# Optimization experiments

Measured on AMD Instinct MI355X. Metric: run time of the kernel, lower is better.

The kernel has to match this reference:

```python
import jax, jax.numpy as jnp
import numpy as np

B, N, H, HS, PH = 8, 384, 12, 768, 64
D = HS // H  # 64


def _ln(x, g, b, eps=1e-5):
    m = jnp.mean(x, axis=-1, keepdims=True)
    v = jnp.mean(jnp.square(x - m), axis=-1, keepdims=True)
    return (x - m) * jax.lax.rsqrt(v + eps) * g + b


def setup_inputs() -> dict:
    key = jax.random.key(0)
    ks = jax.random.split(key, 16)
    s = 0.02
    return {
        "nodes": jax.random.normal(ks[0], (B, N, HS), jnp.float32),
        "bias": jnp.zeros((B, 1, 1, N), jnp.float32),
        "paths": jax.random.normal(ks[1], (B, N, N, PH), jnp.float32),
        "Wq": jax.random.normal(ks[2], (HS, HS), jnp.float32) * s,
        "bq": jnp.zeros((HS,), jnp.float32),
        "Wk": jax.random.normal(ks[3], (HS, HS), jnp.float32) * s,
        "bk": jnp.zeros((HS,), jnp.float32),
        "Wv": jax.random.normal(ks[4], (HS, HS), jnp.float32) * s,
        "bv": jnp.zeros((HS,), jnp.float32),
        "Wsk": jax.random.normal(ks[5], (PH, D), jnp.float32) * s,
        "bsk": jnp.zeros((D,), jnp.float32),
        "Wsv": jax.random.normal(ks[6], (PH, D), jnp.float32) * s,
        "bsv": jnp.zeros((D,), jnp.float32),
        "Wo": jax.random.normal(ks[7], (HS, HS), jnp.float32) * s,
        "bo": jnp.zeros((HS,), jnp.float32),
        "ln_g": jnp.ones((HS,), jnp.float32),
        "ln_b": jnp.zeros((HS,), jnp.float32),
        "pln_g": jnp.ones((PH,), jnp.float32),
        "pln_b": jnp.zeros((PH,), jnp.float32),
    }


def reference(nodes, bias, paths, Wq, bq, Wk, bk, Wv, bv, Wsk, bsk, Wsv, bsv,
              Wo, bo, ln_g, ln_b, pln_g, pln_b):
    # q/k/v projections, split heads -> (B, H, N, D)
    def split(x):
        return x.reshape(B, N, H, D).transpose(0, 2, 1, 3)

    q = split(nodes @ Wq + bq)
    k = split(nodes @ Wk + bk)
    v = split(nodes @ Wv + bv)

    p = _ln(paths, pln_g, pln_b)            # (B, N, N, PH)
    struct_k = p @ Wsk + bsk                # (B, N, N, D)
    struct_v = p @ Wsv + bsv                # (B, N, N, D)

    q = q * (D ** -0.5)
    w = jnp.einsum('bhid,bhjd->bhij', q, k)           # content scores
    w = w + jnp.einsum('bhid,bijd->bhij', q, struct_k)  # structural scores
    w = jax.nn.softmax(w + bias, axis=-1)             # (B, H, N, N)

    out = jnp.einsum('bhij,bhjd->bhid', w, v) \
        + jnp.einsum('bhij,bijd->bhid', w, struct_v)  # (B, H, N, D)
    out = out.transpose(0, 2, 1, 3).reshape(B, N, HS)
    out = jax.nn.relu(out @ Wo + bo)
    # dropout p=0.0 -> identity
    return _ln(nodes + out, ln_g, ln_b), w
```

## Files before the change

### kernel.cpp

```cpp
#include <hip/hip_runtime.h>
#include <hip/hip_bf16.h>

typedef __hip_bfloat16 bf16;
typedef __attribute__((ext_vector_type(8))) short short8b;
typedef __attribute__((ext_vector_type(4))) float f32x4;

#define BB  8
#define NN  384
#define HH  12
#define HSZ 768
#define DD  64
#define PHH 64
#define PSTR 386
#define SWS  194

__device__ __forceinline__ float bflo(unsigned u){ union{unsigned q; float f;} c; c.q = u << 16;        return c.f; }
__device__ __forceinline__ float bfhi(unsigned u){ union{unsigned q; float f;} c; c.q = u & 0xffff0000u; return c.f; }

__device__ __forceinline__ unsigned pk2bf(float lo, float hi){
    union{float f; unsigned u;} a, b; a.f = lo; b.f = hi;
    unsigned ua = a.u + 0x7fffu + ((a.u >> 16) & 1u);
    unsigned ub = b.u + 0x7fffu + ((b.u >> 16) & 1u);
    return (ua >> 16) | (ub & 0xffff0000u);
}

union U8 { uint4 u; short8b v; };

__device__ __forceinline__ void pk32(const float4* p, uint4* o){
    #pragma unroll
    for (int e = 0; e < 4; e++) {
        float4 x = p[2*e], y = p[2*e+1];
        o[e].x = pk2bf(x.x, x.y); o[e].y = pk2bf(x.z, x.w);
        o[e].z = pk2bf(y.x, y.y); o[e].w = pk2bf(y.z, y.w);
    }
}

__global__ __launch_bounds__(256) void k_qkv(
    const float* __restrict__ nodes,
    const float* __restrict__ Wq, const float* __restrict__ bq,
    const float* __restrict__ Wk, const float* __restrict__ bk,
    const float* __restrict__ Wv, const float* __restrict__ bv,
    float* __restrict__ oq, float* __restrict__ okk, float* __restrict__ ov)
{
    const int which = blockIdx.z;
    const float* __restrict__ W   = which==0 ? Wq : (which==1 ? Wk : Wv);
    const float* __restrict__ bia = which==0 ? bq : (which==1 ? bk : bv);
    float* __restrict__ out       = which==0 ? oq : (which==1 ? okk : ov);
    const float scale = which==0 ? 0.125f : 1.0f;

    __shared__ __align__(16) unsigned Alds[128*20];
    __shared__ __align__(16) unsigned Blds[128*20];

    const int row0 = blockIdx.x * 128;
    const int col0 = blockIdx.y * 128;
    const int tid  = threadIdx.x;
    const int wv   = tid >> 6, lane = tid & 63;
    const int wm   = wv & 1,  wn   = wv >> 1;
    const int fr   = lane & 15, kg = lane >> 4;

    f32x4 acc[4][4];
    #pragma unroll
    for (int i=0;i<4;i++){
        #pragma unroll
        for (int j=0;j<4;j++){ acc[i][j][0]=0.f; acc[i][j][1]=0.f; acc[i][j][2]=0.f; acc[i][j][3]=0.f; }
    }

    for (int k0 = 0; k0 < HSZ; k0 += 32) {
        {
            const int m = tid >> 1, kh = tid & 1;
            const float4* ap = reinterpret_cast<const float4*>(nodes + (size_t)(row0 + m)*HSZ + k0 + kh*16);
            float4 a0 = ap[0], a1 = ap[1], a2 = ap[2], a3 = ap[3];
            uint4 p0, p1;
            p0.x = pk2bf(a0.x,a0.y); p0.y = pk2bf(a0.z,a0.w);
            p0.z = pk2bf(a1.x,a1.y); p0.w = pk2bf(a1.z,a1.w);
            p1.x = pk2bf(a2.x,a2.y); p1.y = pk2bf(a2.z,a2.w);
            p1.z = pk2bf(a3.x,a3.y); p1.w = pk2bf(a3.z,a3.w);
            *reinterpret_cast<uint4*>(&Alds[m*20 + kh*8    ]) = p0;
            *reinterpret_cast<uint4*>(&Alds[m*20 + kh*8 + 4]) = p1;
        }
        {
            const int n = tid & 127, kq = tid >> 7;
            const float* wp = W + (size_t)(k0 + kq*16)*HSZ + col0 + n;
            float x[16];
            #pragma unroll
            for (int j = 0; j < 16; j++) x[j] = wp[(size_t)j*HSZ];
            uint4 p0, p1;
            p0.x = pk2bf(x[0],x[1]);   p0.y = pk2bf(x[2],x[3]);
            p0.z = pk2bf(x[4],x[5]);   p0.w = pk2bf(x[6],x[7]);
            p1.x = pk2bf(x[8],x[9]);   p1.y = pk2bf(x[10],x[11]);
            p1.z = pk2bf(x[12],x[13]); p1.w = pk2bf(x[14],x[15]);
            *reinterpret_cast<uint4*>(&Blds[n*20 + kq*8    ]) = p0;
            *reinterpret_cast<uint4*>(&Blds[n*20 + kq*8 + 4]) = p1;
        }
        __syncthreads();
        U8 au[4], bu[4];
        #pragma unroll
        for (int t = 0; t < 4; t++) {
            au[t].u = *reinterpret_cast<const uint4*>(&Alds[(wm*64 + t*16 + fr)*20 + kg*4]);
            bu[t].u = *reinterpret_cast<const uint4*>(&Blds[(wn*64 + t*16 + fr)*20 + kg*4]);
        }
        #pragma unroll
        for (int mt = 0; mt < 4; mt++)
            #pragma unroll
            for (int nt = 0; nt < 4; nt++)
                acc[mt][nt] = __builtin_amdgcn_mfma_f32_16x16x32_bf16(
                    au[mt].v, bu[nt].v, acc[mt][nt], 0, 0, 0);
        __syncthreads();
    }
    #pragma unroll
    for (int nt = 0; nt < 4; nt++) {
        const int col = col0 + wn*64 + nt*16 + fr;
        const int h = col >> 6, d = col & 63;
        const float bv_ = bia[col];
        #pragma unroll
        for (int mt = 0; mt < 4; mt++) {
            #pragma unroll
            for (int r = 0; r < 4; r++) {
                const int m = row0 + wm*64 + mt*16 + kg*4 + r;
                const int b_ = m / NN, n_ = m % NN;
                out[(((size_t)b_*HH + h)*NN + n_)*DD + d] = (acc[mt][nt][r] + bv_) * scale;
            }
        }
    }
}

__global__ __launch_bounds__(256) void k_qsk(
    const float* __restrict__ q_s, const float* __restrict__ Wsk,
    float* __restrict__ qsk)
{
    const int lane = threadIdx.x & 63;
    const int row = blockIdx.x * 4 + (threadIdx.x >> 6);
    const float qd = q_s[(size_t)row * DD + lane];
    float acc = 0.f;
    const float* wr = Wsk + lane * DD;
    #pragma unroll 8
    for (int d = 0; d < DD; d++) acc = fmaf(wr[d], __shfl(qd, d, 64), acc);
    qsk[(size_t)row * DD + lane] = acc;
}

__global__ __launch_bounds__(256) void k_scores(
    const float* __restrict__ q_s, const float* __restrict__ kk_, float* __restrict__ wc)
{
    const int bh = blockIdx.z;
    __shared__ __align__(16) unsigned Alds[128*36];
    __shared__ __align__(16) unsigned Blds[128*36];
    const int i0 = blockIdx.x * 128, j0 = blockIdx.y * 128;
    const int tid = threadIdx.x;
    const int wv  = tid >> 6, lane = tid & 63;
    const int wm  = wv & 1,  wn   = wv >> 1;
    const int fr  = lane & 15, kg = lane >> 4;

    {
        const int m = tid >> 1, kh = tid & 1;
        const float4* ap = reinterpret_cast<const float4*>(q_s + ((size_t)bh*NN + i0 + m)*DD + kh*32);
        const float4* bp = reinterpret_cast<const float4*>(kk_ + ((size_t)bh*NN + j0 + m)*DD + kh*32);
        uint4 pa[4], pbq[4];
        pk32(ap, pa);
        pk32(bp, pbq);
        #pragma unroll
        for (int e = 0; e < 4; e++) {
            *reinterpret_cast<uint4*>(&Alds[m*36 + kh*16 + 4*e]) = pa[e];
            *reinterpret_cast<uint4*>(&Blds[m*36 + kh*16 + 4*e]) = pbq[e];
        }
    }
    __syncthreads();

    f32x4 acc[4][4];
    #pragma unroll
    for (int i=0;i<4;i++){
        #pragma unroll
        for (int j=0;j<4;j++){ acc[i][j][0]=0.f; acc[i][j][1]=0.f; acc[i][j][2]=0.f; acc[i][j][3]=0.f; }
    }
    #pragma unroll
    for (int ks = 0; ks < 2; ks++) {
        U8 au[4], bu[4];
        #pragma unroll
        for (int t = 0; t < 4; t++) {
            au[t].u = *reinterpret_cast<const uint4*>(&Alds[(wm*64 + t*16 + fr)*36 + ks*16 + kg*4]);
            bu[t].u = *reinterpret_cast<const uint4*>(&Blds[(wn*64 + t*16 + fr)*36 + ks*16 + kg*4]);
        }
        #pragma unroll
        for (int mt = 0; mt < 4; mt++)
            #pragma unroll
            for (int nt = 0; nt < 4; nt++)
                acc[mt][nt] = __builtin_amdgcn_mfma_f32_16x16x32_bf16(
                    au[mt].v, bu[nt].v, acc[mt][nt], 0, 0, 0);
    }
    #pragma unroll
    for (int nt = 0; nt < 4; nt++) {
        const int j = j0 + wn*64 + nt*16 + fr;
        #pragma unroll
        for (int mt = 0; mt < 4; mt++) {
            #pragma unroll
            for (int r = 0; r < 4; r++) {
                const int i = i0 + wm*64 + mt*16 + kg*4 + r;
                wc[((size_t)bh*NN + i)*NN + j] = acc[mt][nt][r];
            }
        }
    }
}

__global__ __launch_bounds__(384) void k_soft(
    const float* __restrict__ paths, const float* __restrict__ bias,
    const float* __restrict__ pg, const float* __restrict__ pb,
    const float* __restrict__ wc, const float* __restrict__ qsk,
    float* __restrict__ pagg, float* __restrict__ w_out)
{
    const int bi = blockIdx.x;
    const int b = bi / NN, i = bi % NN;
    __shared__ __align__(16) unsigned pLNT[32 * PSTR];
    __shared__ __align__(16) unsigned sw32[16 * SWS];
    __shared__ __align__(16) unsigned qskA[16 * 36];
    __shared__ float redM[6][16];
    __shared__ float redS[6][16];
    __shared__ float pgf[64], pbf[64];
    const int tid  = threadIdx.x;
    const int wv   = tid >> 6, lane = tid & 63;
    const int g    = lane >> 4, c = lane & 15;
    const int jbase = wv*64 + c;

    float wcv[4][4], biasj[4];
    #pragma unroll
    for (int nt = 0; nt < 4; nt++) {
        const int j = jbase + nt*16;
        biasj[nt] = bias[b*NN + j];
        #pragma unroll
        for (int r = 0; r < 4; r++) {
            const int h = g*4 + r;
            wcv[nt][r] = (h < HH) ? wc[((size_t)(b*HH + h)*NN + i)*NN + j] : 0.f;
        }
    }

    if (tid < 64) { pgf[tid] = pg[tid]; pbf[tid] = pb[tid]; }
    {
        const int h = tid >> 5, t2 = tid & 31;
        const size_t r0 = ((size_t)(b*HH + h)*NN + i)*DD;
        const float q0 = qsk[r0 + 2*t2], q1 = qsk[r0 + 2*t2 + 1];
        qskA[h*36 + t2] = pk2bf(q0, q1);
        if (tid < 144) qskA[432 + tid] = 0u;
    }
    __syncthreads();

    {
        const float4* src = reinterpret_cast<const float4*>(paths + ((size_t)bi * NN + tid) * PHH);
        float x[64];
        #pragma unroll
        for (int t = 0; t < 16; t++) {
            float4 u = src[t];
            x[4*t]=u.x; x[4*t+1]=u.y; x[4*t+2]=u.z; x[4*t+3]=u.w;
        }
        float m0 = 0.f, m1 = 0.f;
        #pragma unroll
        for (int t = 0; t < 32; t++){ m0 += x[2*t]; m1 += x[2*t+1]; }
        const float m = (m0+m1)*(1.f/64.f);
        float v0 = 0.f, v1 = 0.f;
        #pragma unroll
        for (int t = 0; t < 32; t++){
            float a = x[2*t]-m, d = x[2*t+1]-m;
            v0 = fmaf(a,a,v0); v1 = fmaf(d,d,v1);
        }
        const float rs = rsqrtf((v0+v1)*(1.f/64.f) + 1e-5f);
        #pragma unroll
        for (int w = 0; w < 32; w++){
            const float lo = (x[2*w  ]-m)*rs*pgf[2*w  ] + pbf[2*w  ];
            const float hi = (x[2*w+1]-m)*rs*pgf[2*w+1] + pbf[2*w+1];
            pLNT[w*PSTR + tid] = pk2bf(lo, hi);
        }
    }
    __syncthreads();

    f32x4 sc[4];
    #pragma unroll
    for (int nt=0;nt<4;nt++){ sc[nt][0]=0.f; sc[nt][1]=0.f; sc[nt][2]=0.f; sc[nt][3]=0.f; }
    #pragma unroll
    for (int kh = 0; kh < 2; kh++) {
        U8 a; a.u = *reinterpret_cast<const uint4*>(&qskA[c*36 + kh*16 + g*4]);
        #pragma unroll
        for (int nt = 0; nt < 4; nt++) {
            const unsigned* pb_ = &pLNT[(kh*16 + g*4)*PSTR + jbase + nt*16];
            uint4 bw;
            bw.x = pb_[0]; bw.y = pb_[PSTR]; bw.z = pb_[2*PSTR]; bw.w = pb_[3*PSTR];
            U8 bb; bb.u = bw;
            sc[nt] = __builtin_amdgcn_mfma_f32_16x16x32_bf16(a.v, bb.v, sc[nt], 0, 0, 0);
        }
    }
    #pragma unroll
    for (int nt = 0; nt < 4; nt++)
        #pragma unroll
        for (int r = 0; r < 4; r++)
            sc[nt][r] += wcv[nt][r] + biasj[nt];

    float e_[4][4], inv_[4];
    {
        float mr[4];
        #pragma unroll
        for (int r = 0; r < 4; r++) {
            float m2 = fmaxf(fmaxf(sc[0][r], sc[1][r]), fmaxf(sc[2][r], sc[3][r]));
            #pragma unroll
            for (int o = 1; o <= 8; o <<= 1) m2 = fmaxf(m2, __shfl_xor(m2, o, 64));
            mr[r] = m2;
        }
        if (c == 0) {
            #pragma unroll
            for (int r = 0; r < 4; r++) redM[wv][g*4 + r] = mr[r];
        }
        __syncthreads();
        #pragma unroll
        for (int r = 0; r < 4; r++) {
            float Mv = redM[0][g*4 + r];
            #pragma unroll
            for (int w2 = 1; w2 < 6; w2++) Mv = fmaxf(Mv, redM[w2][g*4 + r]);
            float s2 = 0.f;
            #pragma unroll
            for (int nt = 0; nt < 4; nt++){ e_[nt][r] = __expf(sc[nt][r] - Mv); s2 += e_[nt][r]; }
            #pragma unroll
            for (int o = 1; o <= 8; o <<= 1) s2 += __shfl_xor(s2, o, 64);
            mr[r] = s2;
        }
        if (c == 0) {
            #pragma unroll
            for (int r = 0; r < 4; r++) redS[wv][g*4 + r] = mr[r];
        }
        __syncthreads();
        #pragma unroll
        for (int r = 0; r < 4; r++) {
            float Sv = redS[0][g*4 + r];
            #pragma unroll
            for (int w2 = 1; w2 < 6; w2++) Sv += redS[w2][g*4 + r];
            inv_[r] = 1.f / Sv;
        }
    }
    #pragma unroll
    for (int nt = 0; nt < 4; nt++) {
        const int j = jbase + nt*16;
        #pragma unroll
        for (int r = 0; r < 4; r++) {
            const int h = g*4 + r;
            const float wgt = e_[nt][r] * inv_[r];
            if (h < HH) w_out[((size_t)(b*HH + h)*NN + i)*NN + j] = wgt;
            const float oth = __shfl_xor(wgt, 1, 64);
            if ((c & 1) == 0) sw32[h*SWS + (j >> 1)] = pk2bf(wgt, oth);
        }
    }
    __syncthreads();

    if (wv < 4) {
        f32x4 pa; pa[0]=0.f; pa[1]=0.f; pa[2]=0.f; pa[3]=0.f;
        const int prow = 8*wv + (c >> 1);
        const bool hi = (c & 1);
        #pragma unroll 4
        for (int kt = 0; kt < 12; kt++) {
            uint2 a0 = *reinterpret_cast<const uint2*>(&sw32[c*SWS + kt*16 + g*4]);
            uint2 a1 = *reinterpret_cast<const uint2*>(&sw32[c*SWS + kt*16 + g*4 + 2]);
            U8 af; af.u.x = a0.x; af.u.y = a0.y; af.u.z = a1.x; af.u.w = a1.y;
            const unsigned* pr = &pLNT[prow*PSTR + 32*kt + 8*g];
            uint2 w01 = *reinterpret_cast<const uint2*>(&pr[0]);
            uint2 w23 = *reinterpret_cast<const uint2*>(&pr[2]);
            uint2 w45 = *reinterpret_cast<const uint2*>(&pr[4]);
            uint2 w67 = *reinterpret_cast<const uint2*>(&pr[6]);
            uint4 bw;
            if (hi) {
                bw.x = (w01.x >> 16) | (w01.y & 0xffff0000u);
                bw.y = (w23.x >> 16) | (w23.y & 0xffff0000u);
                bw.z = (w45.x >> 16) | (w45.y & 0xffff0000u);
                bw.w = (w67.x >> 16) | (w67.y & 0xffff0000u);
            } else {
                bw.x = (w01.x & 0xffffu) | (w01.y << 16);
                bw.y = (w23.x & 0xffffu) | (w23.y << 16);
                bw.z = (w45.x & 0xffffu) | (w45.y << 16);
                bw.w = (w67.x & 0xffffu) | (w67.y << 16);
            }
            U8 bf_; bf_.u = bw;
            pa = __builtin_amdgcn_mfma_f32_16x16x32_bf16(af.v, bf_.v, pa, 0, 0, 0);
        }
        #pragma unroll
        for (int r = 0; r < 4; r++) {
            const int h = g*4 + r;
            if (h < HH)
                pagg[((size_t)(b*HH + h)*NN + i)*DD + 16*wv + c] = pa[r];
        }
    }
}

__global__ __launch_bounds__(256) void k_av(
    const float* __restrict__ w, const float* __restrict__ v_,
    const float* __restrict__ pagg, const float* __restrict__ Wsv,
    const float* __restrict__ bsv, float* __restrict__ attn)
{
    const int bh = blockIdx.y;
    const int b = bh / HH, h = bh % HH;
    const int i0 = blockIdx.x * 128;
    __shared__ __align__(16) unsigned Alds[128*36];
    __shared__ __align__(16) unsigned Blds[64*36];
    const int tid = threadIdx.x;
    const int wv  = tid >> 6, lane = tid & 63;
    const int fr  = lane & 15, kg = lane >> 4;

    f32x4 acc[2][4];
    #pragma unroll
    for (int i=0;i<2;i++){
        #pragma unroll
        for (int j=0;j<4;j++){ acc[i][j][0]=0.f; acc[i][j][1]=0.f; acc[i][j][2]=0.f; acc[i][j][3]=0.f; }
    }

    for (int step = 0; step < 7; step++) {
        const int j0 = step * 64;
        {
            const int m = tid >> 1, kh = tid & 1;
            const float4* ap = (step < 6)
                ? reinterpret_cast<const float4*>(w    + ((size_t)bh*NN + i0 + m)*NN  + j0 + kh*32)
                : reinterpret_cast<const float4*>(pagg + ((size_t)bh*NN + i0 + m)*PHH + kh*32);
            uint4 pa[4];
            pk32(ap, pa);
            #pragma unroll
            for (int e = 0; e < 4; e++)
                *reinterpret_cast<uint4*>(&Alds[m*36 + kh*16 + 4*e]) = pa[e];
        }
        {
            const int d = tid & 63, kq = tid >> 6;
            const float* vp = (step < 6)
                ? (v_  + ((size_t)bh*NN + j0 + kq*16)*DD + d)
                : (Wsv + (size_t)(kq*16)*DD + d);
            float x[16];
            #pragma unroll
            for (int t = 0; t < 16; t++) x[t] = vp[(size_t)t*DD];
            uint4 p0,p1;
            p0.x=pk2bf(x[0],x[1]);   p0.y=pk2bf(x[2],x[3]);
            p0.z=pk2bf(x[4],x[5]);   p0.w=pk2bf(x[6],x[7]);
            p1.x=pk2bf(x[8],x[9]);   p1.y=pk2bf(x[10],x[11]);
            p1.z=pk2bf(x[12],x[13]); p1.w=pk2bf(x[14],x[15]);
            *reinterpret_cast<uint4*>(&Blds[d*36 + kq*8    ]) = p0;
            *reinterpret_cast<uint4*>(&Blds[d*36 + kq*8 + 4]) = p1;
        }
        __syncthreads();
        #pragma unroll
        for (int ks = 0; ks < 2; ks++) {
            U8 au[2], bu[4];
            #pragma unroll
            for (int mt = 0; mt < 2; mt++)
                au[mt].u = *reinterpret_cast<const uint4*>(&Alds[(wv*32 + mt*16 + fr)*36 + ks*16 + kg*4]);
            #pragma unroll
            for (int nt = 0; nt < 4; nt++)
                bu[nt].u = *reinterpret_cast<const uint4*>(&Blds[(nt*16 + fr)*36 + ks*16 + kg*4]);
            #pragma unroll
            for (int mt = 0; mt < 2; mt++)
                #pragma unroll
                for (int nt = 0; nt < 4; nt++)
                    acc[mt][nt] = __builtin_amdgcn_mfma_f32_16x16x32_bf16(
                        au[mt].v, bu[nt].v, acc[mt][nt], 0, 0, 0);
        }
        __syncthreads();
    }
    #pragma unroll
    for (int nt = 0; nt < 4; nt++) {
        const int d = nt*16 + fr;
        const float bv_ = bsv[d];
        #pragma unroll
        for (int mt = 0; mt < 2; mt++) {
            #pragma unroll
            for (int r = 0; r < 4; r++) {
                const int i = i0 + wv*32 + mt*16 + kg*4 + r;
                attn[((size_t)b*NN + i)*HSZ + h*DD + d] = acc[mt][nt][r] + bv_;
            }
        }
    }
}

__global__ __launch_bounds__(256) void k_proj(
    const float* __restrict__ attn, const float* __restrict__ Wo,
    const float* __restrict__ bo, const float* __restrict__ nodes,
    float* __restrict__ tres)
{
    __shared__ __align__(16) unsigned Alds[128*20];
    __shared__ __align__(16) unsigned Blds[128*20];

    const int row0 = blockIdx.x * 128;
    const int col0 = blockIdx.y * 128;
    const int tid  = threadIdx.x;
    const int wv   = tid >> 6, lane = tid & 63;
    const int wm   = wv & 1,  wn   = wv >> 1;
    const int fr   = lane & 15, kg = lane >> 4;

    f32x4 acc[4][4];
    #pragma unroll
    for (int i=0;i<4;i++){
        #pragma unroll
        for (int j=0;j<4;j++){ acc[i][j][0]=0.f; acc[i][j][1]=0.f; acc[i][j][2]=0.f; acc[i][j][3]=0.f; }
    }

    for (int k0 = 0; k0 < HSZ; k0 += 32) {
        {
            const int m = tid >> 1, kh = tid & 1;
            const float4* ap = reinterpret_cast<const float4*>(attn + (size_t)(row0 + m)*HSZ + k0 + kh*16);
            float4 a0 = ap[0], a1 = ap[1], a2 = ap[2], a3 = ap[3];
            uint4 p0, p1;
            p0.x = pk2bf(a0.x,a0.y); p0.y = pk2bf(a0.z,a0.w);
            p0.z = pk2bf(a1.x,a1.y); p0.w = pk2bf(a1.z,a1.w);
            p1.x = pk2bf(a2.x,a2.y); p1.y = pk2bf(a2.z,a2.w);
            p1.z = pk2bf(a3.x,a3.y); p1.w = pk2bf(a3.z,a3.w);
            *reinterpret_cast<uint4*>(&Alds[m*20 + kh*8    ]) = p0;
            *reinterpret_cast<uint4*>(&Alds[m*20 + kh*8 + 4]) = p1;
        }
        {
            const int n = tid & 127, kq = tid >> 7;
            const float* wp = Wo + (size_t)(k0 + kq*16)*HSZ + col0 + n;
            float x[16];
            #pragma unroll
            for (int j = 0; j < 16; j++) x[j] = wp[(size_t)j*HSZ];
            uint4 p0, p1;
            p0.x = pk2bf(x[0],x[1]);   p0.y = pk2bf(x[2],x[3]);
            p0.z = pk2bf(x[4],x[5]);   p0.w = pk2bf(x[6],x[7]);
            p1.x = pk2bf(x[8],x[9]);   p1.y = pk2bf(x[10],x[11]);
            p1.z = pk2bf(x[12],x[13]); p1.w = pk2bf(x[14],x[15]);
            *reinterpret_cast<uint4*>(&Blds[n*20 + kq*8    ]) = p0;
            *reinterpret_cast<uint4*>(&Blds[n*20 + kq*8 + 4]) = p1;
        }
        __syncthreads();
        U8 au[4], bu[4];
        #pragma unroll
        for (int t = 0; t < 4; t++) {
            au[t].u = *reinterpret_cast<const uint4*>(&Alds[(wm*64 + t*16 + fr)*20 + kg*4]);
            bu[t].u = *reinterpret_cast<const uint4*>(&Blds[(wn*64 + t*16 + fr)*20 + kg*4]);
        }
        #pragma unroll
        for (int mt = 0; mt < 4; mt++)
            #pragma unroll
            for (int nt = 0; nt < 4; nt++)
                acc[mt][nt] = __builtin_amdgcn_mfma_f32_16x16x32_bf16(
                    au[mt].v, bu[nt].v, acc[mt][nt], 0, 0, 0);
        __syncthreads();
    }
    #pragma unroll
    for (int nt = 0; nt < 4; nt++) {
        const int col = col0 + wn*64 + nt*16 + fr;
        const float bov = bo[col];
        #pragma unroll
        for (int mt = 0; mt < 4; mt++) {
            #pragma unroll
            for (int r = 0; r < 4; r++) {
                const int m = row0 + wm*64 + mt*16 + kg*4 + r;
                const float val = fmaxf(acc[mt][nt][r] + bov, 0.f) + nodes[(size_t)m*HSZ + col];
                tres[(size_t)m*HSZ + col] = val;
            }
        }
    }
}

__global__ __launch_bounds__(256) void k_ln(
    const float* __restrict__ tres, const float* __restrict__ g,
    const float* __restrict__ bta, float* __restrict__ out0)
{
    const int row = blockIdx.x;
    const float* x = tres + (size_t)row * HSZ;
    const int tid = threadIdx.x;
    const int wid = tid >> 6, lane = tid & 63;
    __shared__ float r4[4];
    __shared__ float sc[2];
    float v0 = x[tid], v1 = x[tid+256], v2 = x[tid+512];
    float s = v0 + v1 + v2;
    #pragma unroll
    for (int o = 32; o > 0; o >>= 1) s += __shfl_xor(s, o, 64);
    if (lane == 0) r4[wid] = s;
    __syncthreads();
    if (tid == 0) sc[0] = (r4[0]+r4[1]+r4[2]+r4[3]) * (1.f/768.f);
    __syncthreads();
    const float m = sc[0];
    const float d0 = v0-m, d1 = v1-m, d2 = v2-m;
    float vs = d0*d0 + d1*d1 + d2*d2;
    #pragma unroll
    for (int o = 32; o > 0; o >>= 1) vs += __shfl_xor(vs, o, 64);
    if (lane == 0) r4[wid] = vs;
    __syncthreads();
    if (tid == 0) sc[1] = rsqrtf((r4[0]+r4[1]+r4[2]+r4[3]) * (1.f/768.f) + 1e-5f);
    __syncthreads();
    const float rs = sc[1];
    out0[(size_t)row*HSZ + tid      ] = d0*rs*g[tid      ] + bta[tid      ];
    out0[(size_t)row*HSZ + tid + 256] = d1*rs*g[tid + 256] + bta[tid + 256];
    out0[(size_t)row*HSZ + tid + 512] = d2*rs*g[tid + 512] + bta[tid + 512];
}

extern "C" void kernel_launch(void* const* d_in, const int* in_sizes, int n_in,
                              void* d_out, int out_size, void* d_ws, size_t ws_size,
                              hipStream_t stream)
{
    (void)in_sizes; (void)n_in; (void)out_size; (void)ws_size;
    const float* nodes = (const float*)d_in[0];
    const float* bias  = (const float*)d_in[1];
    const float* paths = (const float*)d_in[2];
    const float* Wq = (const float*)d_in[3];
    const float* bq = (const float*)d_in[4];
    const float* Wk = (const float*)d_in[5];
    const float* bk = (const float*)d_in[6];
    const float* Wv = (const float*)d_in[7];
    const float* bv = (const float*)d_in[8];
    const float* Wsk= (const float*)d_in[9];
    const float* Wsv= (const float*)d_in[11];
    const float* bsv= (const float*)d_in[12];
    const float* Wo = (const float*)d_in[13];
    const float* bo = (const float*)d_in[14];
    const float* lng= (const float*)d_in[15];
    const float* lnb= (const float*)d_in[16];
    const float* plg= (const float*)d_in[17];
    const float* plb= (const float*)d_in[18];

    float* ws   = (float*)d_ws;
    float* q_s  = ws;
    float* kbuf = ws + 2359296;
    float* vbuf = ws + 4718592;
    float* qsk  = ws + 7077888;
    float* wc   = ws + 9474048;
    float* attn = q_s;
    float* pagg = kbuf;
    float* tres = wc;

    float* out0 = (float*)d_out;
    float* wout = out0 + (size_t)BB*NN*HSZ;

    hipLaunchKernelGGL(k_qkv,    dim3(24,6,3), dim3(256), 0, stream,
                       nodes, Wq,bq, Wk,bk, Wv,bv, q_s, kbuf, vbuf);
    hipLaunchKernelGGL(k_qsk,    dim3(9216),   dim3(256), 0, stream,
                       q_s, Wsk, qsk);
    hipLaunchKernelGGL(k_scores, dim3(3,3,96), dim3(256), 0, stream,
                       q_s, kbuf, wc);
    hipLaunchKernelGGL(k_soft,   dim3(3072),   dim3(384), 0, stream,
                       paths, bias, plg, plb, wc, qsk, pagg, wout);
    hipLaunchKernelGGL(k_av,     dim3(3,96),   dim3(256), 0, stream,
                       wout, vbuf, pagg, Wsv, bsv, attn);
    hipLaunchKernelGGL(k_proj,   dim3(24,6),   dim3(256), 0, stream,
                       attn, Wo, bo, nodes, tres);
    hipLaunchKernelGGL(k_ln,     dim3(3072),   dim3(256), 0, stream,
                       tres, lng, lnb, out0);
}
```

Measured before the change: 345.7 us.

## Use MFMA for q·Wsk, hoist paths loads, and make LayerNorm one wave per row

```diff
diff --git a/kernel.cpp b/kernel.cpp
--- a/kernel.cpp
+++ b/kernel.cpp
@@ -128,14 +128,68 @@
     const float* __restrict__ q_s, const float* __restrict__ Wsk,
     float* __restrict__ qsk)
 {
-    const int lane = threadIdx.x & 63;
-    const int row = blockIdx.x * 4 + (threadIdx.x >> 6);
-    const float qd = q_s[(size_t)row * DD + lane];
-    float acc = 0.f;
-    const float* wr = Wsk + lane * DD;
-    #pragma unroll 8
-    for (int d = 0; d < DD; d++) acc = fmaf(wr[d], __shfl(qd, d, 64), acc);
-    qsk[(size_t)row * DD + lane] = acc;
+    __shared__ __align__(16) unsigned Alds[128*36];
+    __shared__ __align__(16) unsigned Blds[64*36];
+    const int row0 = blockIdx.x * 128;
+    const int tid = threadIdx.x;
+    const int wv = tid >> 6, lane = tid & 63;
+    const int fr = lane & 15, kg = lane >> 4;
+
+    {
+        const int m = tid >> 1, kh = tid & 1;
+        const float4* ap = reinterpret_cast<const float4*>(q_s + (size_t)(row0 + m)*DD + kh*32);
+        uint4 pa[4]; pk32(ap, pa);
+        #pragma unroll
+        for (int e = 0; e < 4; e++)
+            *reinterpret_cast<uint4*>(&Alds[m*36 + kh*16 + 4*e]) = pa[e];
+    }
+    {
+        const int n = tid & 63, kq = tid >> 6;
+        const float4* bp = reinterpret_cast<const float4*>(Wsk + (size_t)n*DD + kq*16);
+        float4 b0 = bp[0], b1 = bp[1], b2 = bp[2], b3 = bp[3];
+        uint4 p0, p1;
+        p0.x = pk2bf(b0.x,b0.y); p0.y = pk2bf(b0.z,b0.w);
+        p0.z = pk2bf(b1.x,b1.y); p0.w = pk2bf(b1.z,b1.w);
+        p1.x = pk2bf(b2.x,b2.y); p1.y = pk2bf(b2.z,b2.w);
+        p1.z = pk2bf(b3.x,b3.y); p1.w = pk2bf(b3.z,b3.w);
+        *reinterpret_cast<uint4*>(&Blds[n*36 + kq*8    ]) = p0;
+        *reinterpret_cast<uint4*>(&Blds[n*36 + kq*8 + 4]) = p1;
+    }
+    __syncthreads();
+
+    f32x4 acc[2][4];
+    #pragma unroll
+    for (int i=0;i<2;i++){
+        #pragma unroll
+        for (int j=0;j<4;j++){ acc[i][j][0]=0.f; acc[i][j][1]=0.f; acc[i][j][2]=0.f; acc[i][j][3]=0.f; }
+    }
+    #pragma unroll
+    for (int ks = 0; ks < 2; ks++) {
+        U8 au[2], bu[4];
+        #pragma unroll
+        for (int mt = 0; mt < 2; mt++)
+            au[mt].u = *reinterpret_cast<const uint4*>(&Alds[(wv*32 + mt*16 + fr)*36 + ks*16 + kg*4]);
+        #pragma unroll
+        for (int nt = 0; nt < 4; nt++)
+            bu[nt].u = *reinterpret_cast<const uint4*>(&Blds[(nt*16 + fr)*36 + ks*16 + kg*4]);
+        #pragma unroll
+        for (int mt = 0; mt < 2; mt++)
+            #pragma unroll
+            for (int nt = 0; nt < 4; nt++)
+                acc[mt][nt] = __builtin_amdgcn_mfma_f32_16x16x32_bf16(
+                    au[mt].v, bu[nt].v, acc[mt][nt], 0, 0, 0);
+    }
+    #pragma unroll
+    for (int nt = 0; nt < 4; nt++) {
+        #pragma unroll
+        for (int mt = 0; mt < 2; mt++) {
+            #pragma unroll
+            for (int r = 0; r < 4; r++) {
+                const int m = row0 + wv*32 + mt*16 + kg*4 + r;
+                qsk[(size_t)m*DD + nt*16 + fr] = acc[mt][nt][r];
+            }
+        }
+    }
 }
 
 __global__ __launch_bounds__(256) void k_scores(
@@ -219,6 +273,15 @@
     const int g    = lane >> 4, c = lane & 15;
     const int jbase = wv*64 + c;
 
+    float x[64];
+    {
+        const float4* src = reinterpret_cast<const float4*>(paths + ((size_t)bi * NN + tid) * PHH);
+        #pragma unroll
+        for (int t = 0; t < 16; t++) {
+            float4 u = src[t];
+            x[4*t]=u.x; x[4*t+1]=u.y; x[4*t+2]=u.z; x[4*t+3]=u.w;
+        }
+    }
     float wcv[4][4], biasj[4];
     #pragma unroll
     for (int nt = 0; nt < 4; nt++) {
@@ -230,7 +293,6 @@
             wcv[nt][r] = (h < HH) ? wc[((size_t)(b*HH + h)*NN + i)*NN + j] : 0.f;
         }
     }
-
     if (tid < 64) { pgf[tid] = pg[tid]; pbf[tid] = pb[tid]; }
     {
         const int h = tid >> 5, t2 = tid & 31;
@@ -242,13 +304,6 @@
     __syncthreads();
 
     {
-        const float4* src = reinterpret_cast<const float4*>(paths + ((size_t)bi * NN + tid) * PHH);
-        float x[64];
-        #pragma unroll
-        for (int t = 0; t < 16; t++) {
-            float4 u = src[t];
-            x[4*t]=u.x; x[4*t+1]=u.y; x[4*t+2]=u.z; x[4*t+3]=u.w;
-        }
         float m0 = 0.f, m1 = 0.f;
         #pragma unroll
         for (int t = 0; t < 32; t++){ m0 += x[2*t]; m1 += x[2*t+1]; }
@@ -550,33 +605,40 @@
     const float* __restrict__ tres, const float* __restrict__ g,
     const float* __restrict__ bta, float* __restrict__ out0)
 {
-    const int row = blockIdx.x;
-    const float* x = tres + (size_t)row * HSZ;
-    const int tid = threadIdx.x;
-    const int wid = tid >> 6, lane = tid & 63;
-    __shared__ float r4[4];
-    __shared__ float sc[2];
-    float v0 = x[tid], v1 = x[tid+256], v2 = x[tid+512];
-    float s = v0 + v1 + v2;
+    const int row  = blockIdx.x * 4 + (threadIdx.x >> 6);
+    const int lane = threadIdx.x & 63;
+    const float4* x4 = reinterpret_cast<const float4*>(tres + (size_t)row * HSZ);
+    float4 v[3];
+    #pragma unroll
+    for (int t = 0; t < 3; t++) v[t] = x4[lane + t*64];
+    float s = 0.f;
+    #pragma unroll
+    for (int t = 0; t < 3; t++) s += v[t].x + v[t].y + v[t].z + v[t].w;
     #pragma unroll
     for (int o = 32; o > 0; o >>= 1) s += __shfl_xor(s, o, 64);
-    if (lane == 0) r4[wid] = s;
-    __syncthreads();
-    if (tid == 0) sc[0] = (r4[0]+r4[1]+r4[2]+r4[3]) * (1.f/768.f);
-    __syncthreads();
-    const float m = sc[0];
-    const float d0 = v0-m, d1 = v1-m, d2 = v2-m;
-    float vs = d0*d0 + d1*d1 + d2*d2;
+    const float m = s * (1.f/768.f);
+    float vs = 0.f;
+    #pragma unroll
+    for (int t = 0; t < 3; t++) {
+        float a = v[t].x-m, b = v[t].y-m, c = v[t].z-m, d = v[t].w-m;
+        vs += a*a + b*b + c*c + d*d;
+    }
     #pragma unroll
     for (int o = 32; o > 0; o >>= 1) vs += __shfl_xor(vs, o, 64);
-    if (lane == 0) r4[wid] = vs;
-    __syncthreads();
-    if (tid == 0) sc[1] = rsqrtf((r4[0]+r4[1]+r4[2]+r4[3]) * (1.f/768.f) + 1e-5f);
-    __syncthreads();
-    const float rs = sc[1];
-    out0[(size_t)row*HSZ + tid      ] = d0*rs*g[tid      ] + bta[tid      ];
-    out0[(size_t)row*HSZ + tid + 256] = d1*rs*g[tid + 256] + bta[tid + 256];
-    out0[(size_t)row*HSZ + tid + 512] = d2*rs*g[tid + 512] + bta[tid + 512];
+    const float rs = rsqrtf(vs * (1.f/768.f) + 1e-5f);
+    const float4* g4 = reinterpret_cast<const float4*>(g);
+    const float4* b4 = reinterpret_cast<const float4*>(bta);
+    float4* o4 = reinterpret_cast<float4*>(out0 + (size_t)row * HSZ);
+    #pragma unroll
+    for (int t = 0; t < 3; t++) {
+        const int idx = lane + t*64;
+        float4 gg = g4[idx], bb = b4[idx], o;
+        o.x = (v[t].x-m)*rs*gg.x + bb.x;
+        o.y = (v[t].y-m)*rs*gg.y + bb.y;
+        o.z = (v[t].z-m)*rs*gg.z + bb.z;
+        o.w = (v[t].w-m)*rs*gg.w + bb.w;
+        o4[idx] = o;
+    }
 }
 
 extern "C" void kernel_launch(void* const* d_in, const int* in_sizes, int n_in,
@@ -618,7 +680,7 @@
 
     hipLaunchKernelGGL(k_qkv,    dim3(24,6,3), dim3(256), 0, stream,
                        nodes, Wq,bq, Wk,bk, Wv,bv, q_s, kbuf, vbuf);
-    hipLaunchKernelGGL(k_qsk,    dim3(9216),   dim3(256), 0, stream,
+    hipLaunchKernelGGL(k_qsk,    dim3(288),    dim3(256), 0, stream,
                        q_s, Wsk, qsk);
     hipLaunchKernelGGL(k_scores, dim3(3,3,96), dim3(256), 0, stream,
                        q_s, kbuf, wc);
@@ -628,6 +690,6 @@
                        wout, vbuf, pagg, Wsv, bsv, attn);
     hipLaunchKernelGGL(k_proj,   dim3(24,6),   dim3(256), 0, stream,
                        attn, Wo, bo, nodes, tres);
-    hipLaunchKernelGGL(k_ln,     dim3(3072),   dim3(256), 0, stream,
+    hipLaunchKernelGGL(k_ln,     dim3(768),    dim3(256), 0, stream,
                        tres, lng, lnb, out0);
 }
```

Measured after the change: 283.6 us. 18.0% less time.
